# Performance work log

Measured on AMD Instinct MI355X. Metric: run time of the kernel, lower is better.

The kernel has to match this reference:

```python
import jax, jax.numpy as jnp
import numpy as np
from jax import lax

B, D, N, M = 512, 1024, 8192, 2048  # batch, input_dim, n_sdr, n_minicolumns
K = 4            # n_columns
W_SPARSE = 320   # SDR sparsity w (active bits per SDR)
K_ACTIVE = 40    # active minicolumns per step
PERM_THRESH = 0.5
LR = 0.01
CONSENSUS_THRESH = 1.0  # strict AND


def setup_inputs() -> dict:
    key = jax.random.key(0)
    k1, k2, k3 = jax.random.split(key, 3)
    s_batch = jax.random.normal(k1, (B, D), dtype=jnp.float32)
    W_enc = jax.random.normal(k2, (K, D, N), dtype=jnp.float32)  # per-column encoders (no weight sharing)
    perm = jax.random.uniform(k3, (K, M, N), dtype=jnp.float32)  # per-column permanences
    return {"s_batch": s_batch, "W_enc": W_enc, "perm": perm}


def _one_hot_topk(scores, k):
    # scores: [B, C] -> binary [B, C] with top-k per row set to 1
    _, idx = lax.top_k(scores, k)
    rows = jnp.arange(scores.shape[0])[:, None]
    return jnp.zeros_like(scores).at[rows, idx].set(1.0)


def reference(s_batch, W_enc, perm):
    def column(We, P):
        # SDRSpace.encode: random projection + top-w binarization
        scores = s_batch @ We                       # [B, N]
        sdr = _one_hot_topk(scores, W_SPARSE)       # [B, N] binary
        # SpatialPooler.forward_batch: overlap with connected synapses, top-k minicolumns
        connected = (P >= PERM_THRESH).astype(sdr.dtype)  # [M, N]
        overlap = sdr @ connected.T                 # [B, M]
        act = _one_hot_topk(overlap, K_ACTIVE)      # [B, M] binary winners
        # hebbian_update_batch: reinforce active inputs, punish inactive, on winning columns
        delta = (LR / B) * (act.T @ (2.0 * sdr - 1.0))    # [M, N] scatter-accumulated
        P_new = jnp.clip(P + delta, 0.0, 1.0)
        return sdr, P_new

    all_sdrs, perms_new = jax.vmap(column)(W_enc, perm)   # [K,B,N], [K,M,N]
    vote_fraction = all_sdrs.mean(axis=0)                  # [B, N]
    consensus = (vote_fraction >= CONSENSUS_THRESH).astype(jnp.float32)
    return consensus, all_sdrs[0], perms_new
```

## Files before the change

kernel.cpp:

```cpp
#include <hip/hip_runtime.h>
#include <stdint.h>

#define B_   512
#define D_   1024
#define N_   8192
#define M_   2048
#define K_   4
#define WSP  320
#define KACT 40
#define NW   128

typedef _Float16 f16;
typedef _Float16 f16x4 __attribute__((ext_vector_type(4)));
typedef _Float16 f16x8 __attribute__((ext_vector_type(8)));
typedef float f32x4 __attribute__((ext_vector_type(4)));

#define BM 128
#define BN 256
#define SPLIT_SCALE 2048.0f
#define SPLIT_INV (1.0f / 2048.0f)

#define GLD16(g, l) __builtin_amdgcn_global_load_lds( \
    (const __attribute__((address_space(1))) uint32_t*)(g), \
    (__attribute__((address_space(3))) uint32_t*)(l), 16, 0, 0)

__global__ __launch_bounds__(256) void splitS_kernel(const float* __restrict__ S,
                                                     uint8_t* __restrict__ imgA) {
    int blk = blockIdx.x;
    int mt = blk >> 5, dstep = blk & 31;
    int tid = threadIdx.x;
    uint8_t* outb = imgA + (size_t)blk * 16384;
#pragma unroll
    for (int q = 0; q < 4; q++) {
        int o = tid * 16 + q * 4096;
        int r = o >> 7, inner = o & 127;
        int sw = (r & 7) << 4;
        int raw = inner ^ sw;
        int plane = raw >> 6;
        int k0 = (raw & 63) >> 1;
        const float* sp = &S[(size_t)(mt * 128 + r) * D_ + dstep * 32 + k0];
        float4 v0 = *(const float4*)sp;
        float4 v1 = *(const float4*)(sp + 4);
        f16x8 out;
        if (plane == 0) {
            out[0] = (f16)v0.x; out[1] = (f16)v0.y; out[2] = (f16)v0.z; out[3] = (f16)v0.w;
            out[4] = (f16)v1.x; out[5] = (f16)v1.y; out[6] = (f16)v1.z; out[7] = (f16)v1.w;
        } else {
            f16 h0 = (f16)v0.x, h1 = (f16)v0.y, h2 = (f16)v0.z, h3 = (f16)v0.w;
            f16 h4 = (f16)v1.x, h5 = (f16)v1.y, h6 = (f16)v1.z, h7 = (f16)v1.w;
            out[0] = (f16)((v0.x - (float)h0) * SPLIT_SCALE);
            out[1] = (f16)((v0.y - (float)h1) * SPLIT_SCALE);
            out[2] = (f16)((v0.z - (float)h2) * SPLIT_SCALE);
            out[3] = (f16)((v0.w - (float)h3) * SPLIT_SCALE);
            out[4] = (f16)((v1.x - (float)h4) * SPLIT_SCALE);
            out[5] = (f16)((v1.y - (float)h5) * SPLIT_SCALE);
            out[6] = (f16)((v1.z - (float)h6) * SPLIT_SCALE);
            out[7] = (f16)((v1.w - (float)h7) * SPLIT_SCALE);
        }
        *(f16x8*)&outb[o] = out;
    }
}

__device__ __forceinline__ void pack_write_B(uint8_t* Bn, const float* w,
                                             int kc0, int bn, int bsw) {
#pragma unroll
    for (int kci = 0; kci < 2; kci++) {
        int kc = kc0 * 2 + kci;
        f16x8 hv, lv;
#pragma unroll
        for (int j = 0; j < 8; j++) {
            float x = w[kci * 8 + j];
            f16 h = (f16)x;
            hv[j] = h;
            lv[j] = (f16)((x - (float)h) * SPLIT_SCALE);
        }
        *(f16x8*)&Bn[bn * 128 + ((kc * 16) ^ bsw)] = hv;
        *(f16x8*)&Bn[bn * 128 + ((64 + kc * 16) ^ bsw)] = lv;
    }
}

__global__ __launch_bounds__(512, 2) void gemm_kernel(const uint8_t* __restrict__ imgA,
                                                      const float* __restrict__ W,
                                                      float* __restrict__ C) {
    __shared__ __align__(16) uint8_t lds[98304];

    int bid = blockIdx.x;
    int l = (bid & 7) * 64 + (bid >> 3);
    int mt = l & 3, nt = (l >> 2) & 31, kt = l >> 7;

    int tid = threadIdx.x;
    int wave = tid >> 6, lane = tid & 63;
    int wm = wave >> 2, wn = wave & 3;
    int lr = lane & 15, lg = lane >> 4;

    const uint8_t* srcA0 = imgA + (size_t)(mt * 32) * 16384 + wave * 1024 + lane * 16;

    const float* Wp = W + (size_t)kt * D_ * N_ + nt * BN;
    float* Cp = C + (size_t)kt * B_ * N_ + (size_t)(mt * BM) * N_ + nt * BN;

    int bn = tid & 255;
    int kc0 = tid >> 8;
    int bsw = (bn & 7) << 4;

    f32x4 acc0[4][4], acc1[4][4];
#pragma unroll
    for (int i = 0; i < 4; i++)
#pragma unroll
        for (int j = 0; j < 4; j++) {
            acc0[i][j] = (f32x4){0.f, 0.f, 0.f, 0.f};
            acc1[i][j] = (f32x4){0.f, 0.f, 0.f, 0.f};
        }

    {
        uint8_t* dA = lds + wave * 1024;
        GLD16(srcA0, dA);
        GLD16(srcA0 + 8192, dA + 8192);
        float w[16];
        const float* wp0 = Wp + (size_t)(kc0 * 16) * N_ + bn;
#pragma unroll
        for (int j = 0; j < 16; j++) w[j] = wp0[(size_t)j * N_];
        pack_write_B(lds + 32768, w, kc0, bn, bsw);
    }
    __syncthreads();

    for (int dstep = 0; dstep < 32; dstep++) {
        int cur = dstep & 1;
        uint8_t* Ac = lds + cur * 16384;
        uint8_t* Bc = lds + 32768 + cur * 32768;
        bool pf = (dstep < 31);

        float wreg[16];
        if (pf) {
            const uint8_t* sA = srcA0 + (size_t)(dstep + 1) * 16384;
            uint8_t* dA = lds + (cur ^ 1) * 16384 + wave * 1024;
            GLD16(sA, dA);
            GLD16(sA + 8192, dA + 8192);
            const float* wp0 = Wp + (size_t)((dstep + 1) * 32 + kc0 * 16) * N_ + bn;
#pragma unroll
            for (int j = 0; j < 16; j++) wreg[j] = wp0[(size_t)j * N_];
        }

        f16x8 ah[4], al[4];
#pragma unroll
        for (int i = 0; i < 4; i++) {
            int r = wm * 64 + i * 16 + lr;
            int sw = (r & 7) << 4;
            ah[i] = *(const f16x8*)&Ac[r * 128 + ((lg * 16) ^ sw)];
            al[i] = *(const f16x8*)&Ac[r * 128 + ((64 + lg * 16) ^ sw)];
        }
#pragma unroll
        for (int jj = 0; jj < 4; jj++) {
            int n = wn * 64 + jj * 16 + lr;
            int sw = (n & 7) << 4;
            f16x8 bh = *(const f16x8*)&Bc[n * 128 + ((lg * 16) ^ sw)];
            f16x8 bl = *(const f16x8*)&Bc[n * 128 + ((64 + lg * 16) ^ sw)];
            __builtin_amdgcn_s_setprio(1);
#pragma unroll
            for (int i = 0; i < 4; i++) {
                acc0[i][jj] = __builtin_amdgcn_mfma_f32_16x16x32_f16(ah[i], bh, acc0[i][jj], 0, 0, 0);
                acc1[i][jj] = __builtin_amdgcn_mfma_f32_16x16x32_f16(ah[i], bl, acc1[i][jj], 0, 0, 0);
                acc1[i][jj] = __builtin_amdgcn_mfma_f32_16x16x32_f16(al[i], bh, acc1[i][jj], 0, 0, 0);
            }
            __builtin_amdgcn_s_setprio(0);
        }

        if (pf)
            pack_write_B(lds + 32768 + (cur ^ 1) * 32768, wreg, kc0, bn, bsw);

        __syncthreads();
    }

#pragma unroll
    for (int i = 0; i < 4; i++)
#pragma unroll
        for (int jj = 0; jj < 4; jj++) {
            int r0 = wm * 64 + i * 16 + lg * 4;
            int c0 = wn * 64 + jj * 16 + lr;
#pragma unroll
            for (int r = 0; r < 4; r++)
                Cp[(size_t)(r0 + r) * N_ + c0] = acc0[i][jj][r] + acc1[i][jj][r] * SPLIT_INV;
        }
}

__global__ __launch_bounds__(256) void select_conn_kernel(const float* __restrict__ scores,
                                                          uint32_t* __restrict__ sdr_bits32,
                                                          const float* __restrict__ perm,
                                                          uint32_t* __restrict__ conn32,
                                                          int* __restrict__ mcount) {
    int bid = blockIdx.x;
    int tid = threadIdx.x;
    if (bid >= 2048) {
        int km = bid - 2048;
        if (tid == 0) mcount[km] = 0;
        const float* p = perm + (size_t)km * N_ + tid * 32;
        uint32_t bits = 0;
#pragma unroll
        for (int q = 0; q < 8; q++) {
            float4 v = *(const float4*)&p[q * 4];
            bits |= (v.x >= 0.5f ? 1u : 0u) << (q * 4 + 0);
            bits |= (v.y >= 0.5f ? 1u : 0u) << (q * 4 + 1);
            bits |= (v.z >= 0.5f ? 1u : 0u) << (q * 4 + 2);
            bits |= (v.w >= 0.5f ? 1u : 0u) << (q * 4 + 3);
        }
        conn32[(size_t)km * 256 + tid] = bits;
        return;
    }

    __shared__ int hist[256];
    __shared__ int scan2[256];
    __shared__ uint32_t sh_prefix;
    __shared__ int sh_r;

    int kb = bid;
    const float* row = scores + (size_t)kb * N_ + tid * 32;

    uint32_t key[32];
#pragma unroll
    for (int q = 0; q < 8; q++) {
        float4 v = *(const float4*)&row[q * 4];
        uint32_t u0 = __float_as_uint(v.x), u1 = __float_as_uint(v.y);
        uint32_t u2 = __float_as_uint(v.z), u3 = __float_as_uint(v.w);
        key[q * 4 + 0] = (u0 & 0x80000000u) ? ~u0 : (u0 | 0x80000000u);
        key[q * 4 + 1] = (u1 & 0x80000000u) ? ~u1 : (u1 | 0x80000000u);
        key[q * 4 + 2] = (u2 & 0x80000000u) ? ~u2 : (u2 | 0x80000000u);
        key[q * 4 + 3] = (u3 & 0x80000000u) ? ~u3 : (u3 | 0x80000000u);
    }
    if (tid == 0) { sh_prefix = 0u; sh_r = WSP; }
    __syncthreads();

    for (int p = 3; p >= 0; p--) {
        hist[tid] = 0;
        __syncthreads();
        uint32_t prefix = sh_prefix;
        int r = sh_r;
        uint32_t maskHi = (p == 3) ? 0u : (0xFFFFFFFFu << ((p + 1) * 8));
        int shift = p * 8;
#pragma unroll
        for (int j = 0; j < 32; j++) {
            uint32_t u = key[j];
            if ((u & maskHi) == prefix) atomicAdd(&hist[(u >> shift) & 255], 1);
        }
        __syncthreads();
#pragma unroll
        for (int off = 1; off < 256; off <<= 1) {
            int x = hist[tid] + ((tid + off < 256) ? hist[tid + off] : 0);
            __syncthreads();
            hist[tid] = x;
            __syncthreads();
        }
        int Sv = hist[tid];
        int Sn = (tid < 255) ? hist[tid + 1] : 0;
        if (Sv >= r && Sn < r) { sh_prefix = prefix | ((uint32_t)tid << shift); sh_r = r - Sn; }
        __syncthreads();
    }
    uint32_t t = sh_prefix;

    int gt = 0, eq = 0;
#pragma unroll
    for (int j = 0; j < 32; j++) {
        gt += (key[j] > t); eq += (key[j] == t);
    }
    hist[tid] = gt; scan2[tid] = eq;
    __syncthreads();
#pragma unroll
    for (int off = 1; off < 256; off <<= 1) {
        int g = hist[tid] + ((tid >= off) ? hist[tid - off] : 0);
        int e = scan2[tid] + ((tid >= off) ? scan2[tid - off] : 0);
        __syncthreads();
        hist[tid] = g; scan2[tid] = e;
        __syncthreads();
    }
    int totalGt = hist[255];
    int eb = scan2[tid] - eq;
    int r_eq = WSP - totalGt;

    uint32_t bits = 0;
#pragma unroll
    for (int j = 0; j < 32; j++) {
        uint32_t u = key[j];
        bool f = (u > t) || ((u == t) && (eb < r_eq));
        if (u == t) eb++;
        if (f) bits |= (1u << j);
    }
    sdr_bits32[(size_t)kb * 256 + tid] = bits;
}

#define OV_BBLK 16
#define OV_MTILE 512
__global__ __launch_bounds__(256) void overlap_mat_kernel(const uint64_t* __restrict__ sdr_bits,
                                                          const uint64_t* __restrict__ conn,
                                                          uint16_t* __restrict__ ovmat) {
    __shared__ uint64_t sw[OV_BBLK][NW];

    int bid = blockIdx.x;
    int nb = (bid & 7) * 64 + (bid >> 3);
    int k = nb >> 7;
    int rem = nb & 127;
    int b0 = (rem >> 2) * OV_BBLK;
    int m0 = (rem & 3) * OV_MTILE;
    int tid = threadIdx.x;

    for (int i = tid; i < OV_BBLK * NW; i += 256) {
        int bb = i >> 7, w = i & 127;
        sw[bb][w] = sdr_bits[((size_t)k * B_ + b0 + bb) * NW + w];
    }
    __syncthreads();

    int m_a = m0 + tid;
    int m_b = m0 + tid + 256;
    const ulonglong2* cra = (const ulonglong2*)(conn + ((size_t)k * M_ + m_a) * NW);
    const ulonglong2* crb = (const ulonglong2*)(conn + ((size_t)k * M_ + m_b) * NW);

    int acca[OV_BBLK], accb[OV_BBLK];
#pragma unroll
    for (int i = 0; i < OV_BBLK; i++) { acca[i] = 0; accb[i] = 0; }

#pragma unroll 2
    for (int wp = 0; wp < NW / 2; wp++) {
        ulonglong2 ca = cra[wp];
        ulonglong2 cb = crb[wp];
#pragma unroll
        for (int bb = 0; bb < OV_BBLK; bb++) {
            ulonglong2 s = *(const ulonglong2*)&sw[bb][wp * 2];
            acca[bb] += __popcll(ca.x & s.x) + __popcll(ca.y & s.y);
            accb[bb] += __popcll(cb.x & s.x) + __popcll(cb.y & s.y);
        }
    }
#pragma unroll
    for (int bb = 0; bb < OV_BBLK; bb++) {
        ovmat[((size_t)k * B_ + b0 + bb) * M_ + m_a] = (uint16_t)acca[bb];
        ovmat[((size_t)k * B_ + b0 + bb) * M_ + m_b] = (uint16_t)accb[bb];
    }
}

__global__ __launch_bounds__(256) void top40_cons_kernel(const uint16_t* __restrict__ ovmat,
                                                         int* __restrict__ mcount,
                                                         int* __restrict__ mlist,
                                                         const uint64_t* __restrict__ sdr_bits,
                                                         float* __restrict__ cons,
                                                         float* __restrict__ sdr0) {
    int bid = blockIdx.x;
    int tid = threadIdx.x;
    if (bid >= 2048) {
        int gid = (bid - 2048) * 256 + tid;
        int b = gid >> 13;
        int n = gid & (N_ - 1);
        int wi = n >> 6, bit = n & 63;
        size_t base = (size_t)b * NW + wi;
        uint64_t w0 = sdr_bits[base];
        uint64_t w1 = sdr_bits[(size_t)1 * B_ * NW + base];
        uint64_t w2 = sdr_bits[(size_t)2 * B_ * NW + base];
        uint64_t w3 = sdr_bits[(size_t)3 * B_ * NW + base];
        uint64_t a = w0 & w1 & w2 & w3;
        cons[gid] = (float)((a >> bit) & 1);
        sdr0[gid] = (float)((w0 >> bit) & 1);
        return;
    }

    __shared__ int hist[512];
    __shared__ int scanbuf[256];
    __shared__ int sh_t, sh_req;

    int kb = bid;
    int k = kb >> 9;
    int b = kb & 511;

    union { uint4 raw; uint16_t v[8]; } ov;
    ov.raw = *(const uint4*)&ovmat[(size_t)kb * M_ + tid * 8];

    hist[tid] = 0; hist[tid + 256] = 0;
    __syncthreads();
#pragma unroll
    for (int j = 0; j < 8; j++) atomicAdd(&hist[ov.v[j]], 1);
    __syncthreads();
#pragma unroll
    for (int off = 1; off < 512; off <<= 1) {
        int a0 = hist[tid] + ((tid + off < 512) ? hist[tid + off] : 0);
        int a1 = hist[tid + 256] + ((tid + 256 + off < 512) ? hist[tid + 256 + off] : 0);
        __syncthreads();
        hist[tid] = a0; hist[tid + 256] = a1;
        __syncthreads();
    }
#pragma unroll
    for (int which = 0; which < 2; which++) {
        int v = tid + which * 256;
        int Sv = hist[v];
        int Sn = (v < 511) ? hist[v + 1] : 0;
        if (Sv >= KACT && Sn < KACT) { sh_t = v; sh_req = KACT - Sn; }
    }
    __syncthreads();
    int t = sh_t, req = sh_req;
    int eq = 0;
#pragma unroll
    for (int j = 0; j < 8; j++) eq += (ov.v[j] == t);
    scanbuf[tid] = eq;
    __syncthreads();
#pragma unroll
    for (int off = 1; off < 256; off <<= 1) {
        int e = scanbuf[tid] + ((tid >= off) ? scanbuf[tid - off] : 0);
        __syncthreads();
        scanbuf[tid] = e;
        __syncthreads();
    }
    int eb = scanbuf[tid] - eq;
#pragma unroll
    for (int j = 0; j < 8; j++) {
        int m = tid * 8 + j;
        int v2 = ov.v[j];
        bool act = (v2 > t) || (v2 == t && eb < req);
        if (v2 == t) eb++;
        if (act) {
            int pos = atomicAdd(&mcount[k * M_ + m], 1);
            mlist[(((size_t)k * M_ + m) << 9) + pos] = b;
        }
    }
}

__global__ __launch_bounds__(512) void update_kernel(const float* __restrict__ perm,
                                                     const uint64_t* __restrict__ sdr_bits,
                                                     const int* __restrict__ mcount,
                                                     const int* __restrict__ mlist,
                                                     float* __restrict__ pout) {
    __shared__ int blist[512];
    int km = blockIdx.x;
    int k = km / M_;
    int tid = threadIdx.x;
    int cnt = mcount[km];
    for (int i = tid; i < cnt; i += 512) blist[i] = mlist[((size_t)km << 9) + i];
    __syncthreads();

    int n0 = tid * 16;
    int c[16];
#pragma unroll
    for (int j = 0; j < 16; j++) c[j] = 0;
    int wi = n0 >> 6;
    int sh = n0 & 63;
    const uint64_t* sb = sdr_bits + (size_t)k * B_ * NW;
    for (int i = 0; i < cnt; i++) {
        uint64_t wv = sb[(size_t)blist[i] * NW + wi];
        unsigned bits = (unsigned)((wv >> sh) & 0xFFFFu);
#pragma unroll
        for (int j = 0; j < 16; j++) c[j] += (bits >> j) & 1;
    }
    const float scale = (float)(0.01 / 512.0);
    const float* pr = perm + (size_t)km * N_ + n0;
    float* po = pout + (size_t)km * N_ + n0;
#pragma unroll
    for (int q = 0; q < 4; q++) {
        float4 pv = *(const float4*)&pr[q * 4];
        float4 o;
        o.x = fminf(fmaxf(pv.x + scale * (float)(2 * c[q * 4 + 0] - cnt), 0.f), 1.f);
        o.y = fminf(fmaxf(pv.y + scale * (float)(2 * c[q * 4 + 1] - cnt), 0.f), 1.f);
        o.z = fminf(fmaxf(pv.z + scale * (float)(2 * c[q * 4 + 2] - cnt), 0.f), 1.f);
        o.w = fminf(fmaxf(pv.w + scale * (float)(2 * c[q * 4 + 3] - cnt), 0.f), 1.f);
        *(float4*)&po[q * 4] = o;
    }
}

extern "C" void kernel_launch(void* const* d_in, const int* in_sizes, int n_in,
                              void* d_out, int out_size, void* d_ws, size_t ws_size,
                              hipStream_t stream) {
    const float* s_batch = (const float*)d_in[0];
    const float* W_enc   = (const float*)d_in[1];
    const float* perm    = (const float*)d_in[2];

    float* out  = (float*)d_out;
    float* cons = out;
    float* sdr0 = out + (size_t)B_ * N_;
    float* pout = out + (size_t)2 * B_ * N_;

    char* ws = (char*)d_ws;
    float*    scores   = (float*)ws;
    uint16_t* ovmat    = (uint16_t*)ws;
    uint64_t* sdr_bits = (uint64_t*)(ws + ((size_t)64 << 20));
    uint64_t* conn     = (uint64_t*)(ws + ((size_t)66 << 20));
    int*      mcount   = (int*)(ws + ((size_t)74 << 20));
    int*      mlist    = (int*)(ws + ((size_t)75 << 20));
    uint8_t*  imgA     = (uint8_t*)(ws + ((size_t)92 << 20));

    splitS_kernel<<<4 * 32, 256, 0, stream>>>(s_batch, imgA);

    gemm_kernel<<<K_ * (B_ / BM) * (N_ / BN), 512, 0, stream>>>(imgA, W_enc, scores);

    select_conn_kernel<<<2048 + K_ * M_, 256, 0, stream>>>(
        scores, (uint32_t*)sdr_bits, perm, (uint32_t*)conn, mcount);

    overlap_mat_kernel<<<K_ * (B_ / OV_BBLK) * (M_ / OV_MTILE), 256, 0, stream>>>(
        sdr_bits, conn, ovmat);

    top40_cons_kernel<<<2048 + (B_ * N_) / 256, 256, 0, stream>>>(
        ovmat, mcount, mlist, sdr_bits, cons, sdr0);

    update_kernel<<<K_ * M_, 512, 0, stream>>>(perm, sdr_bits, mcount, mlist, pout);
}
```

Measured before the change: 434.9 us.

## Use wave shuffle scans, interleave heavy/light blocks, prefetch rows in update

Swaps the log-step shared-memory scans in the radix top-k select and top-40 kernels for 64-lane wavefront shuffle scans combined across the 4 waves. This removes many __syncthreads barriers per pass. Heavy selection blocks are now interleaved with the light conn-bitpack and consensus blocks (every 5th and every 9th block id), so the heavy ones spread across CUs instead of all launching first. The update kernel's gather loop now software-prefetches 8 SDR words ahead to hide global load latency, at the cost of more registers.

```diff
diff --git a/kernel.cpp b/kernel.cpp
--- a/kernel.cpp
+++ b/kernel.cpp
@@ -189,8 +189,8 @@
                                                           int* __restrict__ mcount) {
     int bid = blockIdx.x;
     int tid = threadIdx.x;
-    if (bid >= 2048) {
-        int km = bid - 2048;
+    if (bid % 5 != 0) {
+        int km = bid - (bid / 5) - 1;
         if (tid == 0) mcount[km] = 0;
         const float* p = perm + (size_t)km * N_ + tid * 32;
         uint32_t bits = 0;
@@ -207,11 +207,13 @@
     }
 
     __shared__ int hist[256];
-    __shared__ int scan2[256];
+    __shared__ int wsum[4];
+    __shared__ int wgt[4];
     __shared__ uint32_t sh_prefix;
     __shared__ int sh_r;
 
-    int kb = bid;
+    int kb = bid / 5;
+    int lane = tid & 63, w = tid >> 6;
     const float* row = scores + (size_t)kb * N_ + tid * 32;
 
     uint32_t key[32];
@@ -226,11 +228,10 @@
         key[q * 4 + 3] = (u3 & 0x80000000u) ? ~u3 : (u3 | 0x80000000u);
     }
     if (tid == 0) { sh_prefix = 0u; sh_r = WSP; }
+    hist[tid] = 0;
     __syncthreads();
 
     for (int p = 3; p >= 0; p--) {
-        hist[tid] = 0;
-        __syncthreads();
         uint32_t prefix = sh_prefix;
         int r = sh_r;
         uint32_t maskHi = (p == 3) ? 0u : (0xFFFFFFFFu << ((p + 1) * 8));
@@ -241,16 +242,22 @@
             if ((u & maskHi) == prefix) atomicAdd(&hist[(u >> shift) & 255], 1);
         }
         __syncthreads();
-#pragma unroll
-        for (int off = 1; off < 256; off <<= 1) {
-            int x = hist[tid] + ((tid + off < 256) ? hist[tid + off] : 0);
-            __syncthreads();
-            hist[tid] = x;
-            __syncthreads();
-        }
-        int Sv = hist[tid];
-        int Sn = (tid < 255) ? hist[tid + 1] : 0;
-        if (Sv >= r && Sn < r) { sh_prefix = prefix | ((uint32_t)tid << shift); sh_r = r - Sn; }
+        int h = hist[tid];
+        int S = h;
+#pragma unroll
+        for (int off = 1; off < 64; off <<= 1) {
+            int t2 = __shfl_down(S, off);
+            if (lane + off < 64) S += t2;
+        }
+        if (lane == 0) wsum[w] = S;
+        __syncthreads();
+        int above = 0;
+#pragma unroll
+        for (int ww = 0; ww < 4; ww++) above += (ww > w) ? wsum[ww] : 0;
+        int G = S + above;
+        int Gn = G - h;
+        if (G >= r && Gn < r) { sh_prefix = prefix | ((uint32_t)tid << shift); sh_r = r - Gn; }
+        hist[tid] = 0;
         __syncthreads();
     }
     uint32_t t = sh_prefix;
@@ -260,18 +267,23 @@
     for (int j = 0; j < 32; j++) {
         gt += (key[j] > t); eq += (key[j] == t);
     }
-    hist[tid] = gt; scan2[tid] = eq;
-    __syncthreads();
-#pragma unroll
-    for (int off = 1; off < 256; off <<= 1) {
-        int g = hist[tid] + ((tid >= off) ? hist[tid - off] : 0);
-        int e = scan2[tid] + ((tid >= off) ? scan2[tid - off] : 0);
-        __syncthreads();
-        hist[tid] = g; scan2[tid] = e;
-        __syncthreads();
-    }
-    int totalGt = hist[255];
-    int eb = scan2[tid] - eq;
+    int eI = eq;
+#pragma unroll
+    for (int off = 1; off < 64; off <<= 1) {
+        int t3 = __shfl_up(eI, off);
+        if (lane >= off) eI += t3;
+    }
+    int gT = gt;
+#pragma unroll
+    for (int off = 1; off < 64; off <<= 1) gT += __shfl_xor(gT, off);
+    if (lane == 63) wsum[w] = eI;
+    if (lane == 0) wgt[w] = gT;
+    __syncthreads();
+    int eqoff = 0;
+#pragma unroll
+    for (int ww = 0; ww < 4; ww++) eqoff += (ww < w) ? wsum[ww] : 0;
+    int totalGt = wgt[0] + wgt[1] + wgt[2] + wgt[3];
+    int eb = eqoff + eI - eq;
     int r_eq = WSP - totalGt;
 
     uint32_t bits = 0;
@@ -341,8 +353,8 @@
                                                          float* __restrict__ sdr0) {
     int bid = blockIdx.x;
     int tid = threadIdx.x;
-    if (bid >= 2048) {
-        int gid = (bid - 2048) * 256 + tid;
+    if (bid % 9 != 0) {
+        int gid = (bid - (bid / 9) - 1) * 256 + tid;
         int b = gid >> 13;
         int n = gid & (N_ - 1);
         int wi = n >> 6, bit = n & 63;
@@ -358,12 +370,13 @@
     }
 
     __shared__ int hist[512];
-    __shared__ int scanbuf[256];
+    __shared__ int wsA[4], wsB[4];
     __shared__ int sh_t, sh_req;
 
-    int kb = bid;
+    int kb = bid / 9;
     int k = kb >> 9;
     int b = kb & 511;
+    int lane = tid & 63, w = tid >> 6;
 
     union { uint4 raw; uint16_t v[8]; } ov;
     ov.raw = *(const uint4*)&ovmat[(size_t)kb * M_ + tid * 8];
@@ -373,36 +386,48 @@
 #pragma unroll
     for (int j = 0; j < 8; j++) atomicAdd(&hist[ov.v[j]], 1);
     __syncthreads();
-#pragma unroll
-    for (int off = 1; off < 512; off <<= 1) {
-        int a0 = hist[tid] + ((tid + off < 512) ? hist[tid + off] : 0);
-        int a1 = hist[tid + 256] + ((tid + 256 + off < 512) ? hist[tid + 256 + off] : 0);
-        __syncthreads();
-        hist[tid] = a0; hist[tid + 256] = a1;
-        __syncthreads();
-    }
-#pragma unroll
-    for (int which = 0; which < 2; which++) {
-        int v = tid + which * 256;
-        int Sv = hist[v];
-        int Sn = (v < 511) ? hist[v + 1] : 0;
-        if (Sv >= KACT && Sn < KACT) { sh_t = v; sh_req = KACT - Sn; }
-    }
+
+    int hL = hist[tid], hH = hist[tid + 256];
+    int SL = hL, SH = hH;
+#pragma unroll
+    for (int off = 1; off < 64; off <<= 1) {
+        int a0 = __shfl_down(SL, off);
+        int a1 = __shfl_down(SH, off);
+        if (lane + off < 64) { SL += a0; SH += a1; }
+    }
+    if (lane == 0) { wsA[w] = SL; wsB[w] = SH; }
+    __syncthreads();
+    int aboveA = 0, aboveB = 0, totH = 0;
+#pragma unroll
+    for (int ww = 0; ww < 4; ww++) {
+        aboveA += (ww > w) ? wsA[ww] : 0;
+        aboveB += (ww > w) ? wsB[ww] : 0;
+        totH += wsB[ww];
+    }
+    int GL = SL + aboveA + totH;
+    int GH = SH + aboveB;
+    int GnL = GL - hL, GnH = GH - hH;
+    if (GL >= KACT && GnL < KACT) { sh_t = tid; sh_req = KACT - GnL; }
+    if (GH >= KACT && GnH < KACT) { sh_t = tid + 256; sh_req = KACT - GnH; }
     __syncthreads();
     int t = sh_t, req = sh_req;
+
     int eq = 0;
 #pragma unroll
     for (int j = 0; j < 8; j++) eq += (ov.v[j] == t);
-    scanbuf[tid] = eq;
-    __syncthreads();
-#pragma unroll
-    for (int off = 1; off < 256; off <<= 1) {
-        int e = scanbuf[tid] + ((tid >= off) ? scanbuf[tid - off] : 0);
-        __syncthreads();
-        scanbuf[tid] = e;
-        __syncthreads();
-    }
-    int eb = scanbuf[tid] - eq;
+    int eI = eq;
+#pragma unroll
+    for (int off = 1; off < 64; off <<= 1) {
+        int t3 = __shfl_up(eI, off);
+        if (lane >= off) eI += t3;
+    }
+    if (lane == 63) wsA[w] = eI;
+    __syncthreads();
+    int eqoff = 0;
+#pragma unroll
+    for (int ww = 0; ww < 4; ww++) eqoff += (ww < w) ? wsA[ww] : 0;
+    int eb = eqoff + eI - eq;
+
 #pragma unroll
     for (int j = 0; j < 8; j++) {
         int m = tid * 8 + j;
@@ -436,12 +461,45 @@
     int wi = n0 >> 6;
     int sh = n0 & 63;
     const uint64_t* sb = sdr_bits + (size_t)k * B_ * NW;
-    for (int i = 0; i < cnt; i++) {
-        uint64_t wv = sb[(size_t)blist[i] * NW + wi];
-        unsigned bits = (unsigned)((wv >> sh) & 0xFFFFu);
-#pragma unroll
-        for (int j = 0; j < 16; j++) c[j] += (bits >> j) & 1;
-    }
+
+#define LDROW(idx) sb[(size_t)blist[idx] * NW + wi]
+#define ACC(x) { unsigned bb_ = (unsigned)(((x) >> sh) & 0xFFFFu); \
+                 _Pragma("unroll") for (int j = 0; j < 16; j++) c[j] += (bb_ >> j) & 1; }
+
+    uint64_t p0 = 0, p1 = 0, p2 = 0, p3 = 0, p4 = 0, p5 = 0, p6 = 0, p7 = 0;
+    if (cnt > 0) p0 = LDROW(0);
+    if (cnt > 1) p1 = LDROW(1);
+    if (cnt > 2) p2 = LDROW(2);
+    if (cnt > 3) p3 = LDROW(3);
+    if (cnt > 4) p4 = LDROW(4);
+    if (cnt > 5) p5 = LDROW(5);
+    if (cnt > 6) p6 = LDROW(6);
+    if (cnt > 7) p7 = LDROW(7);
+
+    for (int base = 0; base < cnt; base += 8) {
+        uint64_t c0 = p0, c1 = p1, c2 = p2, c3 = p3, c4 = p4, c5 = p5, c6 = p6, c7 = p7;
+        int nx = base + 8;
+        if (nx + 0 < cnt) p0 = LDROW(nx + 0);
+        if (nx + 1 < cnt) p1 = LDROW(nx + 1);
+        if (nx + 2 < cnt) p2 = LDROW(nx + 2);
+        if (nx + 3 < cnt) p3 = LDROW(nx + 3);
+        if (nx + 4 < cnt) p4 = LDROW(nx + 4);
+        if (nx + 5 < cnt) p5 = LDROW(nx + 5);
+        if (nx + 6 < cnt) p6 = LDROW(nx + 6);
+        if (nx + 7 < cnt) p7 = LDROW(nx + 7);
+        int nv = cnt - base;
+        ACC(c0);
+        if (nv > 1) ACC(c1);
+        if (nv > 2) ACC(c2);
+        if (nv > 3) ACC(c3);
+        if (nv > 4) ACC(c4);
+        if (nv > 5) ACC(c5);
+        if (nv > 6) ACC(c6);
+        if (nv > 7) ACC(c7);
+    }
+#undef LDROW
+#undef ACC
+
     const float scale = (float)(0.01 / 512.0);
     const float* pr = perm + (size_t)km * N_ + n0;
     float* po = pout + (size_t)km * N_ + n0;
@@ -482,13 +540,13 @@
 
     gemm_kernel<<<K_ * (B_ / BM) * (N_ / BN), 512, 0, stream>>>(imgA, W_enc, scores);
 
-    select_conn_kernel<<<2048 + K_ * M_, 256, 0, stream>>>(
+    select_conn_kernel<<<2048 * 5, 256, 0, stream>>>(
         scores, (uint32_t*)sdr_bits, perm, (uint32_t*)conn, mcount);
 
     overlap_mat_kernel<<<K_ * (B_ / OV_BBLK) * (M_ / OV_MTILE), 256, 0, stream>>>(
         sdr_bits, conn, ovmat);
 
-    top40_cons_kernel<<<2048 + (B_ * N_) / 256, 256, 0, stream>>>(
+    top40_cons_kernel<<<2048 * 9, 256, 0, stream>>>(
         ovmat, mcount, mlist, sdr_bits, cons, sdr0);
 
     update_kernel<<<K_ * M_, 512, 0, stream>>>(perm, sdr_bits, mcount, mlist, pout);
```

Result: no change. 428.2 us (-1.6%).
